# Kernel optimization log

Hardware: AMD Instinct MI355X
Metric: run time of the kernel (lower is better)

Reference implementation:

```python
import jax, jax.numpy as jnp
import numpy as np

THRESH = 0.5  # global `thresh` used by ActFun (NOT init_thresh)
LENS = 0.5    # global `lens` (surrogate window)
DECAY = 0.25  # init_decay


@jax.custom_vjp
def act_fun(u):
    return (u > THRESH).astype(u.dtype)

def _act_fwd(u):
    return act_fun(u), u

def _act_bwd(u, g):
    surrogate = (jnp.abs(u - THRESH) < LENS).astype(g.dtype) / (2.0 * LENS)
    return (g * surrogate,)

act_fun.defvjp(_act_fwd, _act_bwd)


def setup_inputs() -> dict:
    key = jax.random.key(0)
    x = jax.random.normal(key, (32, 256, 4096), dtype=jnp.float32)  # [T, B, D]
    return {"x": x}


def reference(x):
    # LIF recurrence: mem_t = mem_{t-1} * decay * (1 - stop_grad(spike_{t-1})) + x_t
    mem0 = x[0]
    spike0 = act_fun(mem0)

    def step(carry, x_t):
        mem, spike = carry
        mem = mem * DECAY * (1.0 - jax.lax.stop_gradient(spike)) + x_t
        s = act_fun(mem)
        return (mem, s), s

    _, spikes = jax.lax.scan(step, (mem0, spike0), x[1:])
    return jnp.concatenate([spike0[None], spikes], axis=0)  # [T, B, D]
```

## Files before the change

kernel.cpp:

```cpp
#include <hip/hip_runtime.h>


constexpr int   T_STEPS = 32;
constexpr int   CHUNK   = 8;
constexpr float THRESH  = 0.5f;
constexpr float DECAY   = 0.25f;

typedef float v4f __attribute__((ext_vector_type(4)));

__device__ __forceinline__ void load_chunk(float4* buf, const float4* __restrict__ xp,
                                           int t0, int n4) {
#pragma unroll
    for (int k = 0; k < CHUNK; ++k)
        buf[k] = xp[(t0 + k) * n4];
}

template <int T0>
__device__ __forceinline__ void compute_chunk(const float4* buf, float4& mem, float4& s,
                                              float4* __restrict__ op, int n4) {
#pragma unroll
    for (int k = 0; k < CHUNK; ++k) {
        float4 v = buf[k];
        if (T0 + k == 0) {
            mem = v;
        } else {
            mem.x = mem.x * (DECAY * (1.0f - s.x)) + v.x;
            mem.y = mem.y * (DECAY * (1.0f - s.y)) + v.y;
            mem.z = mem.z * (DECAY * (1.0f - s.z)) + v.z;
            mem.w = mem.w * (DECAY * (1.0f - s.w)) + v.w;
        }
        s.x = mem.x > THRESH ? 1.0f : 0.0f;
        s.y = mem.y > THRESH ? 1.0f : 0.0f;
        s.z = mem.z > THRESH ? 1.0f : 0.0f;
        s.w = mem.w > THRESH ? 1.0f : 0.0f;
        v4f sv = {s.x, s.y, s.z, s.w};
        __builtin_nontemporal_store(sv, (v4f*)(op + (T0 + k) * n4));
    }
}

__global__ __launch_bounds__(256) void lif_fwd_kernel(
    const float4* __restrict__ x,
    float4* __restrict__ out,
    int n4)
{
    int i = blockIdx.x * 256 + threadIdx.x;
    if (i >= n4) return;

    const float4* xp = x + i;
    float4*       op = out + i;

    float4 bufA[CHUNK], bufB[CHUNK];
    float4 mem, s;

    load_chunk(bufA, xp, 0, n4);
    load_chunk(bufB, xp, 8, n4);
    compute_chunk<0>(bufA, mem, s, op, n4);
    load_chunk(bufA, xp, 16, n4);
    compute_chunk<8>(bufB, mem, s, op, n4);
    load_chunk(bufB, xp, 24, n4);
    compute_chunk<16>(bufA, mem, s, op, n4);
    compute_chunk<24>(bufB, mem, s, op, n4);
}

extern "C" void kernel_launch(void* const* d_in, const int* in_sizes, int n_in,
                              void* d_out, int out_size, void* d_ws, size_t ws_size,
                              hipStream_t stream) {
    const float* x = (const float*)d_in[0];
    float* out = (float*)d_out;

    const int total = in_sizes[0];
    const int n     = total / T_STEPS;
    const int n4    = n / 4;

    const int block = 256;
    const int grid  = (n4 + block - 1) / block;

    lif_fwd_kernel<<<grid, block, 0, stream>>>(
        reinterpret_cast<const float4*>(x),
        reinterpret_cast<float4*>(out),
        n4);
}
```

Before: 230.9 us.

## Stage input chunks through LDS with direct global-to-LDS loads

Replaces the register double-buffered chunk loads with per-chunk global_load_lds transfers into shared memory, followed by a block barrier and compute reading from LDS. This is meant to cut VGPR pressure and raise occupancy so more waves hide memory latency. In exchange it loses the explicit load/compute overlap within a thread and adds a barrier per chunk. The bounds check was also removed.

```diff
diff --git a/kernel.cpp b/kernel.cpp
--- a/kernel.cpp
+++ b/kernel.cpp
@@ -8,58 +8,55 @@
 
 typedef float v4f __attribute__((ext_vector_type(4)));
 
-__device__ __forceinline__ void load_chunk(float4* buf, const float4* __restrict__ xp,
-                                           int t0, int n4) {
-#pragma unroll
-    for (int k = 0; k < CHUNK; ++k)
-        buf[k] = xp[(t0 + k) * n4];
-}
-
-template <int T0>
-__device__ __forceinline__ void compute_chunk(const float4* buf, float4& mem, float4& s,
-                                              float4* __restrict__ op, int n4) {
-#pragma unroll
-    for (int k = 0; k < CHUNK; ++k) {
-        float4 v = buf[k];
-        if (T0 + k == 0) {
-            mem = v;
-        } else {
-            mem.x = mem.x * (DECAY * (1.0f - s.x)) + v.x;
-            mem.y = mem.y * (DECAY * (1.0f - s.y)) + v.y;
-            mem.z = mem.z * (DECAY * (1.0f - s.z)) + v.z;
-            mem.w = mem.w * (DECAY * (1.0f - s.w)) + v.w;
-        }
-        s.x = mem.x > THRESH ? 1.0f : 0.0f;
-        s.y = mem.y > THRESH ? 1.0f : 0.0f;
-        s.z = mem.z > THRESH ? 1.0f : 0.0f;
-        s.w = mem.w > THRESH ? 1.0f : 0.0f;
-        v4f sv = {s.x, s.y, s.z, s.w};
-        __builtin_nontemporal_store(sv, (v4f*)(op + (T0 + k) * n4));
-    }
-}
-
 __global__ __launch_bounds__(256) void lif_fwd_kernel(
     const float4* __restrict__ x,
     float4* __restrict__ out,
     int n4)
 {
-    int i = blockIdx.x * 256 + threadIdx.x;
-    if (i >= n4) return;
+    __shared__ float4 smem[CHUNK][4][64];
+
+    const int tid  = threadIdx.x;
+    const int wave = tid >> 6;
+    const int lane = tid & 63;
+    const int i    = blockIdx.x * 256 + tid;
 
     const float4* xp = x + i;
     float4*       op = out + i;
 
-    float4 bufA[CHUNK], bufB[CHUNK];
     float4 mem, s;
 
-    load_chunk(bufA, xp, 0, n4);
-    load_chunk(bufB, xp, 8, n4);
-    compute_chunk<0>(bufA, mem, s, op, n4);
-    load_chunk(bufA, xp, 16, n4);
-    compute_chunk<8>(bufB, mem, s, op, n4);
-    load_chunk(bufB, xp, 24, n4);
-    compute_chunk<16>(bufA, mem, s, op, n4);
-    compute_chunk<24>(bufB, mem, s, op, n4);
+    for (int c = 0; c < T_STEPS / CHUNK; ++c) {
+        const int t0 = c * CHUNK;
+
+#pragma unroll
+        for (int k = 0; k < CHUNK; ++k) {
+            __builtin_amdgcn_global_load_lds(
+                (const __attribute__((address_space(1))) void*)(xp + (t0 + k) * n4),
+                (__attribute__((address_space(3))) void*)(&smem[k][wave][0]),
+                16, 0, 0);
+        }
+
+        __syncthreads();
+
+#pragma unroll
+        for (int k = 0; k < CHUNK; ++k) {
+            float4 v = smem[k][wave][lane];
+            if (t0 + k == 0) {
+                mem = v;
+            } else {
+                mem.x = mem.x * (DECAY * (1.0f - s.x)) + v.x;
+                mem.y = mem.y * (DECAY * (1.0f - s.y)) + v.y;
+                mem.z = mem.z * (DECAY * (1.0f - s.z)) + v.z;
+                mem.w = mem.w * (DECAY * (1.0f - s.w)) + v.w;
+            }
+            s.x = mem.x > THRESH ? 1.0f : 0.0f;
+            s.y = mem.y > THRESH ? 1.0f : 0.0f;
+            s.z = mem.z > THRESH ? 1.0f : 0.0f;
+            s.w = mem.w > THRESH ? 1.0f : 0.0f;
+            v4f sv = {s.x, s.y, s.z, s.w};
+            __builtin_nontemporal_store(sv, (v4f*)(op + (t0 + k) * n4));
+        }
+    }
 }
 
 extern "C" void kernel_launch(void* const* d_in, const int* in_sizes, int n_in,
```

Result: slower. 236.0 us (+2.2%).
